# Optimization experiments

Hardware: AMD Instinct MI355X
Metric: run time of the kernel (lower is better)

## Reference

```python
import jax, jax.numpy as jnp
import numpy as np

NEG = -1000000.0  # mask fill value used by the torch module

def setup_inputs() -> dict:
    key = jax.random.key(0)
    ks = jax.random.split(key, 7)
    B, Tq, Tk, Din, H, Dv = 16, 128, 256, 64, 256, 256
    return {
        "queries": jax.random.normal(ks[0], (B, Tq, Din), dtype=jnp.float32),
        "keys": jax.random.normal(ks[1], (B, Tk, Din), dtype=jnp.float32),
        "values": jax.random.normal(ks[2], (B, Tk, Dv), dtype=jnp.float32),
        "valid_lens": jax.random.randint(ks[3], (B,), 0, Tk, dtype=jnp.int32),
        "wq": jax.random.normal(ks[4], (Din, H), dtype=jnp.float32) * 0.05,
        "wk": jax.random.normal(ks[5], (Din, H), dtype=jnp.float32) * 0.05,
        "wv": jax.random.normal(ks[6], (H,), dtype=jnp.float32) * 0.05,
    }

def reference(queries, keys, values, valid_lens, wq, wk, wv):
    # Project queries and keys to num_hiddens
    q = jnp.einsum("bqd,dh->bqh", queries, wq)       # [B,Tq,H]
    k = jnp.einsum("bkd,dh->bkh", keys, wk)          # [B,Tk,H]
    # Additive features [B,Tq,Tk,H] -> tanh -> scalar score via wv
    feats = jnp.tanh(q[:, :, None, :] + k[:, None, :, :])
    scores = jnp.einsum("bqkh,h->bqk", feats, wv)    # [B,Tq,Tk]
    # Masked softmax over last axis; valid_lens [B] broadcasts over Tq
    Tk = scores.shape[-1]
    mask = jnp.arange(Tk)[None, None, :] < valid_lens[:, None, None]
    scores = jnp.where(mask, scores, NEG)
    attn = jax.nn.softmax(scores, axis=-1)           # [B,Tq,Tk]
    return jnp.einsum("bqk,bkv->bqv", attn, values)  # [B,Tq,Dv]
```

## Files before the change

kernel.cpp:

```cpp
#include <hip/hip_runtime.h>

#define B_  16
#define TQ  128
#define TK  256
#define DIN 64
#define H_  256
#define DV  256
#define HT  8
#define QT  2
#define NEG -1000000.0f

#define SCALE  2.8853900817779268f
#define LOG2E  1.4426950408889634f

__device__ inline float fast_exp2(float x) { return __builtin_amdgcn_exp2f(x); }
__device__ inline float fast_rcp(float x)  { return __builtin_amdgcn_rcpf(x); }

__global__ __launch_bounds__(256) void proj_k_kernel(
    const float* __restrict__ keys, const float* __restrict__ wk,
    float* __restrict__ kpT, const int* __restrict__ valid_lens)
{
    int b  = blockIdx.x >> 5;
    int h0 = (blockIdx.x & 31) * HT;
    int t  = threadIdx.x;
    int vlC = (valid_lens[b] + 63) & ~63;
    if (t >= vlC) return;
    const float* krow = keys + (b * TK + t) * DIN;
    float acc[HT];
    #pragma unroll
    for (int hh = 0; hh < HT; ++hh) acc[hh] = 0.f;
    #pragma unroll 4
    for (int d = 0; d < DIN; ++d) {
        float kv = krow[d];
        #pragma unroll
        for (int hh = 0; hh < HT; ++hh)
            acc[hh] = fmaf(kv, wk[d * H_ + h0 + hh], acc[hh]);
    }
    #pragma unroll
    for (int hh = 0; hh < HT; ++hh)
        kpT[(b * H_ + h0 + hh) * TK + t] = acc[hh] * SCALE;
}

__device__ inline float waveMax(float v) {
    #pragma unroll
    for (int off = 32; off > 0; off >>= 1) v = fmaxf(v, __shfl_xor(v, off, 64));
    return v;
}
__device__ inline float waveSum(float v) {
    #pragma unroll
    for (int off = 32; off > 0; off >>= 1) v += __shfl_xor(v, off, 64);
    return v;
}

__global__ __launch_bounds__(512) void attn_kernel(
    const float* __restrict__ queries, const float* __restrict__ wq,
    const float* __restrict__ kpT,
    const float* __restrict__ values, const int* __restrict__ valid_lens,
    const float* __restrict__ wv, float* __restrict__ out)
{
    __shared__ float4 qw4[H_];
    __shared__ float  scoreP[2][QT][TK];
    __shared__ float2 attnT[TK];

    int bx   = blockIdx.x;
    int xcd  = bx & 7;
    int i    = bx >> 3;
    int b    = xcd + 8 * (i & 1);
    int q0   = (i >> 1) * QT;
    int t    = threadIdx.x;
    int half = t >> 8;
    int lo   = t & 255;
    int vl   = valid_lens[b];

    if (t < 256) {
        const float* qbase = queries + (b * TQ + q0) * DIN;
        float a0 = 0.f, a1 = 0.f;
        #pragma unroll
        for (int d = 0; d < DIN; ++d) {
            float w = wq[d * H_ + t];
            a0 = fmaf(qbase[d],       w, a0);
            a1 = fmaf(qbase[DIN + d], w, a1);
        }
        qw4[t] = make_float4(a0 * SCALE, a1 * SCALE, wv[t], 0.f);
    }
    __syncthreads();

    if ((lo & 192) < vl) {
        const float* kcol = kpT + b * H_ * TK + lo;
        int h0 = half * (H_ / 2);
        float s0 = 0.f, s1 = 0.f;
        #pragma unroll 4
        for (int hh = 0; hh < H_ / 2; ++hh) {
            int h = h0 + hh;
            float  kv = kcol[h * TK];
            float4 qv = qw4[h];
            float u0 = qv.x + kv, u1 = qv.y + kv;
            float r0 = fast_rcp(fast_exp2(u0) + 1.f);
            float r1 = fast_rcp(fast_exp2(u1) + 1.f);
            s0 = fmaf(qv.z, fmaf(-2.f, r0, 1.f), s0);
            s1 = fmaf(qv.z, fmaf(-2.f, r1, 1.f), s1);
        }
        scoreP[half][0][lo] = s0;
        scoreP[half][1][lo] = s1;
    }
    __syncthreads();

    if (t < 64 * QT) {
        int w    = t >> 6;
        int lane = t & 63;
        float v0 = scoreP[0][w][lane      ] + scoreP[1][w][lane      ];
        float v1 = scoreP[0][w][lane +  64] + scoreP[1][w][lane +  64];
        float v2 = scoreP[0][w][lane + 128] + scoreP[1][w][lane + 128];
        float v3 = scoreP[0][w][lane + 192] + scoreP[1][w][lane + 192];
        v0 = (lane       < vl) ? v0 : NEG;
        v1 = (lane +  64 < vl) ? v1 : NEG;
        v2 = (lane + 128 < vl) ? v2 : NEG;
        v3 = (lane + 192 < vl) ? v3 : NEG;
        float m  = waveMax(fmaxf(fmaxf(v0, v1), fmaxf(v2, v3)));
        float p0 = fast_exp2((v0 - m) * LOG2E);
        float p1 = fast_exp2((v1 - m) * LOG2E);
        float p2 = fast_exp2((v2 - m) * LOG2E);
        float p3 = fast_exp2((v3 - m) * LOG2E);
        float dr = fast_rcp(waveSum(p0 + p1 + p2 + p3));
        ((float*)&attnT[lane      ])[w] = p0 * dr;
        ((float*)&attnT[lane +  64])[w] = p1 * dr;
        ((float*)&attnT[lane + 128])[w] = p2 * dr;
        ((float*)&attnT[lane + 192])[w] = p3 * dr;
    }
    __syncthreads();

    {
        int kLim = (vl == 0) ? TK : vl;
        int k0   = half * (TK / 2);
        int kEnd = min(k0 + TK / 2, kLim);
        const float* vcol = values + b * TK * DV + lo;
        float o0 = 0.f, o1 = 0.f;
        #pragma unroll 4
        for (int k = k0; k < kEnd; ++k) {
            float  vv = vcol[k * DV];
            float2 a  = attnT[k];
            o0 = fmaf(a.x, vv, o0);
            o1 = fmaf(a.y, vv, o1);
        }
        if (half == 1) {
            scoreP[1][0][lo] = o0;
            scoreP[1][1][lo] = o1;
        }
        __syncthreads();
        if (half == 0) {
            float* orow = out + (b * TQ + q0) * DV + lo;
            orow[0]  = o0 + scoreP[1][0][lo];
            orow[DV] = o1 + scoreP[1][1][lo];
        }
    }
}

extern "C" void kernel_launch(void* const* d_in, const int* in_sizes, int n_in,
                              void* d_out, int out_size, void* d_ws, size_t ws_size,
                              hipStream_t stream) {
    const float* queries    = (const float*)d_in[0];
    const float* keys       = (const float*)d_in[1];
    const float* values     = (const float*)d_in[2];
    const int*   valid_lens = (const int*)  d_in[3];
    const float* wq         = (const float*)d_in[4];
    const float* wk         = (const float*)d_in[5];
    const float* wv         = (const float*)d_in[6];
    float* out = (float*)d_out;

    float* kpT = (float*)d_ws;

    proj_k_kernel<<<B_ * (H_ / HT), 256, 0, stream>>>(keys, wk, kpT, valid_lens);
    attn_kernel<<<B_ * (TQ / QT), 512, 0, stream>>>(queries, wq, kpT, values,
                                                    valid_lens, wv, out);
}
```

Before: 115.3 us.

## Register-tile additive scores over 4 queries and 4 keys per thread

Each block now handles four query rows instead of two. In the score phase, each thread computes a 4-key by 4-query tile from one float4 load of projected keys, and the 8 waves split the hidden dimension, with partial sums reduced in shared memory. This raises reuse of each key load and each LDS read, and the grid shrinks by half. In exchange it drops the per-64-key valid-length skip in the score phase, so masked keys are now scored too, and shared-memory use grows.

Result: no change. 114.7 us (-0.6%).

```diff
diff --git a/kernel.cpp b/kernel.cpp
--- a/kernel.cpp
+++ b/kernel.cpp
@@ -7,7 +7,8 @@
 #define H_  256
 #define DV  256
 #define HT  8
-#define QT  2
+#define QT  4
+#define NW  8
 #define NEG -1000000.0f
 
 #define SCALE  2.8853900817779268f
@@ -52,105 +53,134 @@
     return v;
 }
 
+#define ROW4(qr, sacc)                                            \
+    {                                                             \
+        float u0 = (qr) + kv.x, u1 = (qr) + kv.y;                 \
+        float u2 = (qr) + kv.z, u3 = (qr) + kv.w;                 \
+        float r0 = fast_rcp(fast_exp2(u0) + 1.f);                 \
+        float r1 = fast_rcp(fast_exp2(u1) + 1.f);                 \
+        float r2 = fast_rcp(fast_exp2(u2) + 1.f);                 \
+        float r3 = fast_rcp(fast_exp2(u3) + 1.f);                 \
+        sacc.x = fmaf(wvh, fmaf(-2.f, r0, 1.f), sacc.x);          \
+        sacc.y = fmaf(wvh, fmaf(-2.f, r1, 1.f), sacc.y);          \
+        sacc.z = fmaf(wvh, fmaf(-2.f, r2, 1.f), sacc.z);          \
+        sacc.w = fmaf(wvh, fmaf(-2.f, r3, 1.f), sacc.w);          \
+    }
+
 __global__ __launch_bounds__(512) void attn_kernel(
     const float* __restrict__ queries, const float* __restrict__ wq,
     const float* __restrict__ kpT,
     const float* __restrict__ values, const int* __restrict__ valid_lens,
     const float* __restrict__ wv, float* __restrict__ out)
 {
-    __shared__ float4 qw4[H_];
-    __shared__ float  scoreP[2][QT][TK];
-    __shared__ float2 attnT[TK];
-
-    int bx   = blockIdx.x;
-    int xcd  = bx & 7;
-    int i    = bx >> 3;
-    int b    = xcd + 8 * (i & 1);
-    int q0   = (i >> 1) * QT;
-    int t    = threadIdx.x;
-    int half = t >> 8;
-    int lo   = t & 255;
-    int vl   = valid_lens[b];
-
-    if (t < 256) {
-        const float* qbase = queries + (b * TQ + q0) * DIN;
+    __shared__ float2 qs2[2][H_];
+    __shared__ float  wvL[H_];
+    __shared__ float  scoreP[NW][QT][TK];
+    __shared__ float  attnT[TK][QT];
+
+    int bx = blockIdx.x;
+    int xcd = bx & 7;
+    int i   = bx >> 3;
+    int b   = xcd + 8 * (i & 1);
+    int q0  = (i >> 1) * QT;
+    int t   = threadIdx.x;
+    int w   = t >> 6, l = t & 63;
+    int vl  = valid_lens[b];
+
+    {
+        int h = t & 255, rp = t >> 8;
+        const float* qbase = queries + (b * TQ + q0 + rp * 2) * DIN;
         float a0 = 0.f, a1 = 0.f;
         #pragma unroll
         for (int d = 0; d < DIN; ++d) {
-            float w = wq[d * H_ + t];
-            a0 = fmaf(qbase[d],       w, a0);
-            a1 = fmaf(qbase[DIN + d], w, a1);
-        }
-        qw4[t] = make_float4(a0 * SCALE, a1 * SCALE, wv[t], 0.f);
+            float ww = wq[d * H_ + h];
+            a0 = fmaf(qbase[d],       ww, a0);
+            a1 = fmaf(qbase[DIN + d], ww, a1);
+        }
+        qs2[rp][h] = make_float2(a0 * SCALE, a1 * SCALE);
+        if (t < 256) wvL[h] = wv[h];
     }
     __syncthreads();
 
-    if ((lo & 192) < vl) {
-        const float* kcol = kpT + b * H_ * TK + lo;
-        int h0 = half * (H_ / 2);
-        float s0 = 0.f, s1 = 0.f;
+    {
+        const float4* kp4 = (const float4*)(kpT + (size_t)b * H_ * TK);
+        float4 s0 = {0,0,0,0}, s1 = {0,0,0,0}, s2 = {0,0,0,0}, s3 = {0,0,0,0};
+        int h0 = w * (H_ / NW);
+        #pragma unroll 2
+        for (int hh = 0; hh < H_ / NW; ++hh) {
+            int h = h0 + hh;
+            float4 kv  = kp4[h * (TK / 4) + l];
+            float2 qA  = qs2[0][h];
+            float2 qB  = qs2[1][h];
+            float  wvh = wvL[h];
+            ROW4(qA.x, s0);
+            ROW4(qA.y, s1);
+            ROW4(qB.x, s2);
+            ROW4(qB.y, s3);
+        }
+        ((float4*)&scoreP[w][0][0])[l] = s0;
+        ((float4*)&scoreP[w][1][0])[l] = s1;
+        ((float4*)&scoreP[w][2][0])[l] = s2;
+        ((float4*)&scoreP[w][3][0])[l] = s3;
+    }
+    __syncthreads();
+
+    if (t < 64 * QT) {
+        int r = w;
+        float4 v = {0,0,0,0};
+        #pragma unroll
+        for (int s = 0; s < NW; ++s) {
+            float4 ps = ((const float4*)&scoreP[s][r][0])[l];
+            v.x += ps.x; v.y += ps.y; v.z += ps.z; v.w += ps.w;
+        }
+        int k0 = 4 * l;
+        v.x = (k0     < vl) ? v.x : NEG;
+        v.y = (k0 + 1 < vl) ? v.y : NEG;
+        v.z = (k0 + 2 < vl) ? v.z : NEG;
+        v.w = (k0 + 3 < vl) ? v.w : NEG;
+        float m  = waveMax(fmaxf(fmaxf(v.x, v.y), fmaxf(v.z, v.w)));
+        float p0 = fast_exp2((v.x - m) * LOG2E);
+        float p1 = fast_exp2((v.y - m) * LOG2E);
+        float p2 = fast_exp2((v.z - m) * LOG2E);
+        float p3 = fast_exp2((v.w - m) * LOG2E);
+        float dr = fast_rcp(waveSum(p0 + p1 + p2 + p3));
+        attnT[k0    ][r] = p0 * dr;
+        attnT[k0 + 1][r] = p1 * dr;
+        attnT[k0 + 2][r] = p2 * dr;
+        attnT[k0 + 3][r] = p3 * dr;
+    }
+    __syncthreads();
+
+    {
+        int half = t >> 8, v = t & 255;
+        int kLim = (vl == 0) ? TK : vl;
+        int kBeg = half * (TK / 2);
+        int kEnd = min(kBeg + TK / 2, kLim);
+        const float*  vcol = values + (size_t)b * TK * DV + v;
+        const float4* at4  = (const float4*)attnT;
+        float o0 = 0.f, o1 = 0.f, o2 = 0.f, o3 = 0.f;
         #pragma unroll 4
-        for (int hh = 0; hh < H_ / 2; ++hh) {
-            int h = h0 + hh;
-            float  kv = kcol[h * TK];
-            float4 qv = qw4[h];
-            float u0 = qv.x + kv, u1 = qv.y + kv;
-            float r0 = fast_rcp(fast_exp2(u0) + 1.f);
-            float r1 = fast_rcp(fast_exp2(u1) + 1.f);
-            s0 = fmaf(qv.z, fmaf(-2.f, r0, 1.f), s0);
-            s1 = fmaf(qv.z, fmaf(-2.f, r1, 1.f), s1);
-        }
-        scoreP[half][0][lo] = s0;
-        scoreP[half][1][lo] = s1;
-    }
-    __syncthreads();
-
-    if (t < 64 * QT) {
-        int w    = t >> 6;
-        int lane = t & 63;
-        float v0 = scoreP[0][w][lane      ] + scoreP[1][w][lane      ];
-        float v1 = scoreP[0][w][lane +  64] + scoreP[1][w][lane +  64];
-        float v2 = scoreP[0][w][lane + 128] + scoreP[1][w][lane + 128];
-        float v3 = scoreP[0][w][lane + 192] + scoreP[1][w][lane + 192];
-        v0 = (lane       < vl) ? v0 : NEG;
-        v1 = (lane +  64 < vl) ? v1 : NEG;
-        v2 = (lane + 128 < vl) ? v2 : NEG;
-        v3 = (lane + 192 < vl) ? v3 : NEG;
-        float m  = waveMax(fmaxf(fmaxf(v0, v1), fmaxf(v2, v3)));
-        float p0 = fast_exp2((v0 - m) * LOG2E);
-        float p1 = fast_exp2((v1 - m) * LOG2E);
-        float p2 = fast_exp2((v2 - m) * LOG2E);
-        float p3 = fast_exp2((v3 - m) * LOG2E);
-        float dr = fast_rcp(waveSum(p0 + p1 + p2 + p3));
-        ((float*)&attnT[lane      ])[w] = p0 * dr;
-        ((float*)&attnT[lane +  64])[w] = p1 * dr;
-        ((float*)&attnT[lane + 128])[w] = p2 * dr;
-        ((float*)&attnT[lane + 192])[w] = p3 * dr;
-    }
-    __syncthreads();
-
-    {
-        int kLim = (vl == 0) ? TK : vl;
-        int k0   = half * (TK / 2);
-        int kEnd = min(k0 + TK / 2, kLim);
-        const float* vcol = values + b * TK * DV + lo;
-        float o0 = 0.f, o1 = 0.f;
-        #pragma unroll 4
-        for (int k = k0; k < kEnd; ++k) {
+        for (int k = kBeg; k < kEnd; ++k) {
             float  vv = vcol[k * DV];
-            float2 a  = attnT[k];
+            float4 a  = at4[k];
             o0 = fmaf(a.x, vv, o0);
             o1 = fmaf(a.y, vv, o1);
+            o2 = fmaf(a.z, vv, o2);
+            o3 = fmaf(a.w, vv, o3);
         }
         if (half == 1) {
-            scoreP[1][0][lo] = o0;
-            scoreP[1][1][lo] = o1;
+            scoreP[0][0][v] = o0;
+            scoreP[0][1][v] = o1;
+            scoreP[0][2][v] = o2;
+            scoreP[0][3][v] = o3;
         }
         __syncthreads();
         if (half == 0) {
-            float* orow = out + (b * TQ + q0) * DV + lo;
-            orow[0]  = o0 + scoreP[1][0][lo];
-            orow[DV] = o1 + scoreP[1][1][lo];
+            float* orow = out + (size_t)(b * TQ + q0) * DV + v;
+            orow[0]      = o0 + scoreP[0][0][v];
+            orow[DV]     = o1 + scoreP[0][1][v];
+            orow[2 * DV] = o2 + scoreP[0][2][v];
+            orow[3 * DV] = o3 + scoreP[0][3][v];
         }
     }
 }
```
